# Kernel tuning notes

Hardware: AMD Instinct MI355X
Metric: run time of the kernel (lower is better)

The kernel has to match this reference:

```python
import jax, jax.numpy as jnp
import numpy as np

D_MODEL = 1024
N_HEADS = 16
HEAD_DIM = D_MODEL // N_HEADS


def setup_inputs() -> dict:
    key = jax.random.key(0)
    ks = jax.random.split(key, 10)
    s = 1.0 / np.sqrt(D_MODEL)
    inp = {
        "ts_features": jax.random.normal(ks[0], (8, 512, D_MODEL), dtype=jnp.float32),
        "llm_features": jax.random.normal(ks[1], (8, 2048, D_MODEL), dtype=jnp.float32),
        "q_w": jax.random.uniform(ks[2], (D_MODEL, D_MODEL), jnp.float32, -s, s),
        "q_b": jax.random.uniform(ks[3], (D_MODEL,), jnp.float32, -s, s),
        "k_w": jax.random.uniform(ks[4], (D_MODEL, D_MODEL), jnp.float32, -s, s),
        "k_b": jax.random.uniform(ks[5], (D_MODEL,), jnp.float32, -s, s),
        "v_w": jax.random.uniform(ks[6], (D_MODEL, D_MODEL), jnp.float32, -s, s),
        "v_b": jax.random.uniform(ks[7], (D_MODEL,), jnp.float32, -s, s),
        "o_w": jax.random.uniform(ks[8], (D_MODEL, D_MODEL), jnp.float32, -s, s),
        "o_b": jax.random.uniform(ks[9], (D_MODEL,), jnp.float32, -s, s),
    }
    return inp


def reference(ts_features, llm_features, q_w, q_b, k_w, k_b, v_w, v_b, o_w, o_b):
    B, P, _ = ts_features.shape
    S = llm_features.shape[1]
    # Linear projections (torch Linear: x @ W^T + b); split heads -> [B, H, L, Dh]
    q = (ts_features @ q_w.T + q_b).reshape(B, P, N_HEADS, HEAD_DIM).transpose(0, 2, 1, 3)
    k = (llm_features @ k_w.T + k_b).reshape(B, S, N_HEADS, HEAD_DIM).transpose(0, 2, 1, 3)
    v = (llm_features @ v_w.T + v_b).reshape(B, S, N_HEADS, HEAD_DIM).transpose(0, 2, 1, 3)
    # Full attention: scores [B, H, P, S]
    scores = jnp.einsum("bhpd,bhsd->bhps", q, k) / np.sqrt(HEAD_DIM).astype(np.float32)
    attn = jax.nn.softmax(scores, axis=-1)  # dropout is identity in eval mode
    context = jnp.einsum("bhps,bhsd->bhpd", attn, v)
    context = context.transpose(0, 2, 1, 3).reshape(B, P, D_MODEL)
    return context @ o_w.T + o_b
```

## Files before the change

### kernel.cpp

```cpp
#include <hip/hip_runtime.h>

#define DM 1024
#define B_ 8
#define P_ 512
#define S_ 2048

typedef __bf16 bf16;
typedef __bf16 bf16x4 __attribute__((ext_vector_type(4)));
typedef __bf16 bf16x8 __attribute__((ext_vector_type(8)));
typedef float f32x4 __attribute__((ext_vector_type(4)));
typedef float f32x16 __attribute__((ext_vector_type(16)));

__device__ __forceinline__ void gload_lds16(const void* g, void* l) {
  __builtin_amdgcn_global_load_lds(
      (const __attribute__((address_space(1))) unsigned int*)g,
      (__attribute__((address_space(3))) unsigned int*)l, 16, 0, 0);
}

__device__ __forceinline__ f32x4 mfma16(bf16x8 a, bf16x8 b, f32x4 c) {
  return __builtin_amdgcn_mfma_f32_16x16x32_bf16(a, b, c, 0, 0, 0);
}
__device__ __forceinline__ f32x16 mfma32(bf16x8 a, bf16x8 b, f32x16 c) {
  return __builtin_amdgcn_mfma_f32_32x32x16_bf16(a, b, c, 0, 0, 0);
}

__device__ __forceinline__ unsigned cvt_pk_bf16(float lo, float hi) {
  unsigned r;
  asm("v_cvt_pk_bf16_f32 %0, %1, %2" : "=v"(r) : "v"(lo), "v"(hi));
  return r;
}
__device__ __forceinline__ void plswap(unsigned& a, unsigned& b) {
  asm volatile("s_nop 1\n\tv_permlane32_swap_b32 %0, %1" : "+v"(a), "+v"(b));
}
__device__ __forceinline__ void bar() {
  asm volatile("" ::: "memory");
  __builtin_amdgcn_s_barrier();
  asm volatile("" ::: "memory");
}

union U8 { unsigned u[4]; bf16x8 v; };

#define QSCALE 0.18033688011112042f

__global__ void cvt_kernel(const float* __restrict__ in, bf16* __restrict__ out, int n4) {
  int i = blockIdx.x * blockDim.x + threadIdx.x;
  int stride = gridDim.x * blockDim.x;
  for (; i < n4; i += stride) {
    float4 v = reinterpret_cast<const float4*>(in)[i];
    bf16x4 o;
    o[0] = (bf16)v.x; o[1] = (bf16)v.y; o[2] = (bf16)v.z; o[3] = (bf16)v.w;
    reinterpret_cast<bf16x4*>(out)[i] = o;
  }
}

enum { MODE_F32 = 0, MODE_Q = 1, MODE_K = 2, MODE_VT = 3 };

template <int MODE>
__global__ __launch_bounds__(256) void gemm_bt(
    const bf16* __restrict__ A, const bf16* __restrict__ Bw,
    const float* __restrict__ bias, void* __restrict__ out) {
  __shared__ char As[16384];
  __shared__ char Bs[16384];
  const int tid = threadIdx.x;
  const int w = tid >> 6, lane = tid & 63;
  const int g = lane >> 4, l15 = lane & 15;
  const int tn = blockIdx.x, tm = blockIdx.y;
  const int wm = w >> 1, wn = w & 1;

  f32x4 acc[4][4] = {};

  const char* Abase = (const char*)A + (size_t)(tm * 128) * (DM * 2);
  const char* Bbase = (const char*)Bw + (size_t)(tn * 128) * (DM * 2);

  for (int kt = 0; kt < DM / 64; ++kt) {
#pragma unroll
    for (int i = 0; i < 4; ++i) {
      int f = (w * 4 + i) * 1024 + lane * 16;
      int row = f >> 7;
      int kb = f & 127;
      int src = kb ^ ((row & 7) << 4);
      gload_lds16(Abase + (size_t)row * (DM * 2) + kt * 128 + src, As + (w * 4 + i) * 1024);
      gload_lds16(Bbase + (size_t)row * (DM * 2) + kt * 128 + src, Bs + (w * 4 + i) * 1024);
    }
    __syncthreads();
#pragma unroll
    for (int kk = 0; kk < 2; ++kk) {
      bf16x8 af[4], bfr[4];
#pragma unroll
      for (int mi = 0; mi < 4; ++mi) {
        int row = wm * 64 + mi * 16 + l15;
        int off = row * 128 + ((kk * 64 + g * 16) ^ ((row & 7) << 4));
        af[mi] = *reinterpret_cast<const bf16x8*>(As + off);
      }
#pragma unroll
      for (int ni = 0; ni < 4; ++ni) {
        int row = wn * 64 + ni * 16 + l15;
        int off = row * 128 + ((kk * 64 + g * 16) ^ ((row & 7) << 4));
        bfr[ni] = *reinterpret_cast<const bf16x8*>(Bs + off);
      }
#pragma unroll
      for (int mi = 0; mi < 4; ++mi)
#pragma unroll
        for (int ni = 0; ni < 4; ++ni)
          acc[mi][ni] = mfma16(af[mi], bfr[ni], acc[mi][ni]);
    }
    __syncthreads();
  }

#pragma unroll
  for (int mi = 0; mi < 4; ++mi) {
#pragma unroll
    for (int ni = 0; ni < 4; ++ni) {
      const int n = tn * 128 + wn * 64 + ni * 16 + l15;
      const float bn = bias[n];
      const int mb = tm * 128 + wm * 64 + mi * 16 + g * 4;
#pragma unroll
      for (int r = 0; r < 4; ++r) {
        const int m = mb + r;
        const float v = acc[mi][ni][r] + bn;
        if constexpr (MODE == MODE_F32) {
          ((float*)out)[(size_t)m * 1024 + n] = v;
        } else {
          const int b = m >> 9, p = m & 511, h = n >> 6, d = n & 63;
          ((bf16*)out)[((size_t)((b * 16 + h) * 512 + p)) * 64 + d] = (bf16)(v * QSCALE);
        }
      }
    }
  }
}

template <int MODE>
__global__ __launch_bounds__(512, 2) void gemm256(
    const bf16* __restrict__ A, const bf16* __restrict__ Bw,
    const float* __restrict__ bias, void* __restrict__ out) {
  __shared__ char lds[131072];
  const int tid = threadIdx.x;
  const int w = tid >> 6, lane = tid & 63;
  const int g = lane >> 4, l15 = lane & 15;
  const int wm = w >> 2, wn = w & 3;

  const int id = blockIdx.x;
  const int nid = (id & 7) * 32 + (id >> 3);
  const int tn = nid & 3, tm = nid >> 2;

  const int f0 = tid * 16, f1 = f0 + 8192;
  const int r0 = f0 >> 7, r1 = f1 >> 7;
  const size_t so0 = (size_t)r0 * 2048 + ((f0 & 127) ^ ((r0 & 7) << 4));
  const size_t so1 = (size_t)r1 * 2048 + ((f1 & 127) ^ ((r1 & 7) << 4));

  const char* Ab = (const char*)A + (size_t)(tm * 256) * 2048;
  const char* Bb = (const char*)Bw + (size_t)(tn * 256) * 2048;

#define STG(OP, HALF, KT)                                                      \
  {                                                                            \
    const char* base = ((OP) ? Bb : Ab) + (size_t)((HALF) * 128) * 2048 +      \
                       (size_t)(KT) * 128;                                     \
    char* dst = lds + (OP) * 65536 + ((((KT) & 1) * 2 + (HALF)) * 16384);      \
    gload_lds16(base + so0, dst + f0);                                         \
    gload_lds16(base + so1, dst + f1);                                         \
  }

  f32x4 acc[8][4] = {};
  bf16x8 a[4][2], b0[2][2], b1[2][2];

#define RD_A(MH)                                                               \
  _Pragma("unroll") for (int mi = 0; mi < 4; ++mi) _Pragma("unroll")           \
      for (int kk = 0; kk < 2; ++kk) {                                         \
    int lr = (MH) * 64 + mi * 16 + l15;                                        \
    int off = (((unsigned)(kt & 1) * 2 + wm) * 16384) + lr * 128 +             \
              ((kk * 64 + g * 16) ^ ((lr & 7) << 4));                          \
    a[mi][kk] = *reinterpret_cast<const bf16x8*>(lds + off);                   \
  }
#define RD_B(NH, DST)                                                          \
  _Pragma("unroll") for (int ni = 0; ni < 2; ++ni) _Pragma("unroll")           \
      for (int kk = 0; kk < 2; ++kk) {                                         \
    int lr = (wn & 1) * 64 + ((NH) * 2 + ni) * 16 + l15;                       \
    int off = 65536 + (((unsigned)(kt & 1) * 2 + (wn >> 1)) * 16384) +         \
              lr * 128 + ((kk * 64 + g * 16) ^ ((lr & 7) << 4));               \
    DST[ni][kk] = *reinterpret_cast<const bf16x8*>(lds + off);                 \
  }
#define MM(MH, NH, B)                                                          \
  __builtin_amdgcn_s_setprio(1);                                              \
  _Pragma("unroll") for (int mi = 0; mi < 4; ++mi) _Pragma("unroll")           \
      for (int ni = 0; ni < 2; ++ni) _Pragma("unroll")                         \
      for (int kk = 0; kk < 2; ++kk)                                           \
          acc[(MH)*4 + mi][(NH)*2 + ni] =                                      \
              mfma16(a[mi][kk], B[ni][kk], acc[(MH)*4 + mi][(NH)*2 + ni]);     \
  __builtin_amdgcn_s_setprio(0);

  STG(0, 0, 0); STG(1, 0, 0); STG(0, 1, 0); STG(1, 1, 0);
  STG(1, 1, 1); STG(0, 0, 1); STG(1, 0, 1);
  asm volatile("s_waitcnt vmcnt(6)" ::: "memory");
  bar();

  for (int kt = 0; kt < 16; ++kt) {
    RD_A(0); RD_B(0, b0);
    if (kt + 1 < 16) STG(0, 1, kt + 1);
    bar();
    MM(0, 0, b0);
    bar();
    RD_B(1, b1);
    bar();
    MM(0, 1, b1);
    bar();
    RD_A(1);
    if (kt + 2 < 16) STG(1, 1, kt + 2);
    bar();
    MM(1, 0, b0);
    bar();
    if (kt + 2 < 16) { STG(0, 0, kt + 2); STG(1, 0, kt + 2); }
    if (kt < 14) {
      asm volatile("s_waitcnt vmcnt(6)" ::: "memory");
    } else {
      asm volatile("s_waitcnt vmcnt(0)" ::: "memory");
    }
    bar();
    MM(1, 1, b1);
    bar();
  }

#pragma unroll
  for (int am = 0; am < 8; ++am) {
#pragma unroll
    for (int an = 0; an < 4; ++an) {
      const int n = tn * 256 + wn * 64 + an * 16 + l15;
      const float bn = bias[n];
      const int mb = tm * 256 + wm * 128 + am * 16 + g * 4;
      const int h = n >> 6, d = n & 63;
      if constexpr (MODE == MODE_VT) {
        const int b = mb >> 11, s = mb & 2047;
        bf16x4 pk;
#pragma unroll
        for (int r = 0; r < 4; ++r) pk[r] = (bf16)(acc[am][an][r] + bn);
        *reinterpret_cast<bf16x4*>((bf16*)out + ((size_t)((b * 16 + h) * 64 + d)) * 2048 + s) = pk;
      } else {
#pragma unroll
        for (int r = 0; r < 4; ++r) {
          const int m = mb + r;
          const int b = m >> 11, s = m & 2047;
          ((bf16*)out)[((size_t)((b * 16 + h) * 2048 + s)) * 64 + d] =
              (bf16)(acc[am][an][r] + bn);
        }
      }
    }
  }
#undef STG
#undef RD_A
#undef RD_B
#undef MM
}

__global__ __launch_bounds__(256) void attn_kernel(
    const bf16* __restrict__ Q, const bf16* __restrict__ K,
    const bf16* __restrict__ VT, bf16* __restrict__ ctx) {
  __shared__ char lds[32768];
  const int tid = threadIdx.x;
  const int w = tid >> 6, lane = tid & 63;
  const int l31 = lane & 31, hi = lane >> 5;

  const int n = blockIdx.x;
  const int xcd = n & 7, mm = n >> 3;
  const int bh = xcd + ((mm >> 2) << 3);
  const int qt = mm & 3;
  const int q0 = qt * 128;

  const char* Kb = (const char*)(K + (size_t)bh * 2048 * 64);
  const char* Vb = (const char*)(VT + (size_t)bh * 64 * 2048);

  const char* Qrow = (const char*)(Q + ((size_t)bh * 512 + q0 + w * 32 + l31) * 64);
  bf16x8 qf[4];
#pragma unroll
  for (int kk = 0; kk < 4; ++kk)
    qf[kk] = *reinterpret_cast<const bf16x8*>(Qrow + kk * 32 + hi * 16);

  float lrun = 0.f;
  f32x16 oacc[2] = {};

#define STAGE(S0, BUF)                                                        \
  {                                                                           \
    _Pragma("unroll") for (int i = 0; i < 2; ++i) {                           \
      int f = i * 4096 + (w * 64 + lane) * 16;                                \
      int row = f >> 7, bb = f & 127;                                         \
      int src = bb ^ ((row & 7) << 4);                                        \
      gload_lds16(Kb + (size_t)((S0) + row) * 128 + src,                      \
                  (BUF) + i * 4096 + w * 1024);                               \
      gload_lds16(Vb + (size_t)row * 4096 + (size_t)(S0) * 2 + src,           \
                  (BUF) + 8192 + i * 4096 + w * 1024);                        \
    }                                                                         \
  }

  STAGE(0, lds);

  for (int c = 0; c < 32; ++c) {
    char* cur = lds + (c & 1) * 16384;
    if (c + 1 < 32) {
      STAGE((c + 1) * 64, lds + ((c + 1) & 1) * 16384);
      asm volatile("s_waitcnt vmcnt(4)" ::: "memory");
    } else {
      asm volatile("s_waitcnt vmcnt(0)" ::: "memory");
    }
    bar();

    f32x16 sa[2] = {};
    __builtin_amdgcn_s_setprio(1);
#pragma unroll
    for (int t = 0; t < 2; ++t) {
#pragma unroll
      for (int kk = 0; kk < 4; ++kk) {
        int row = t * 32 + l31;
        int off = row * 128 + ((kk * 32 + hi * 16) ^ ((row & 7) << 4));
        bf16x8 kf = *reinterpret_cast<const bf16x8*>(cur + off);
        sa[t] = mfma32(kf, qf[kk], sa[t]);
      }
    }
    __builtin_amdgcn_s_setprio(0);

    bf16x8 pf[4];
#pragma unroll
    for (int t = 0; t < 2; ++t)
#pragma unroll
      for (int h2 = 0; h2 < 2; ++h2) {
        float p[8];
#pragma unroll
        for (int j = 0; j < 8; ++j) {
          p[j] = __builtin_amdgcn_exp2f(sa[t][8 * h2 + j]);
          lrun += p[j];
        }
        unsigned a0 = cvt_pk_bf16(p[0], p[1]);
        unsigned a1 = cvt_pk_bf16(p[2], p[3]);
        unsigned a2 = cvt_pk_bf16(p[4], p[5]);
        unsigned a3 = cvt_pk_bf16(p[6], p[7]);
        plswap(a0, a2);
        plswap(a1, a3);
        U8 u;
        u.u[0] = a0; u.u[1] = a1; u.u[2] = a2; u.u[3] = a3;
        pf[t * 2 + h2] = u.v;
      }

    __builtin_amdgcn_s_setprio(1);
#pragma unroll
    for (int dt = 0; dt < 2; ++dt) {
#pragma unroll
      for (int ks = 0; ks < 4; ++ks) {
        int row = dt * 32 + l31;
        int off = 8192 + row * 128 + ((ks * 32 + hi * 16) ^ ((row & 7) << 4));
        bf16x8 vf = *reinterpret_cast<const bf16x8*>(cur + off);
        oacc[dt] = mfma32(vf, pf[ks], oacc[dt]);
      }
    }
    __builtin_amdgcn_s_setprio(0);
    bar();
  }

  lrun += __shfl_xor(lrun, 32);
  const float inv = 1.0f / lrun;
  const int b = bh >> 4, h = bh & 15;
  const int prow = q0 + w * 32 + l31;
  bf16* dst = ctx + ((size_t)(b * 512 + prow)) * 1024 + h * 64;
#pragma unroll
  for (int dt = 0; dt < 2; ++dt)
#pragma unroll
    for (int g4 = 0; g4 < 4; ++g4) {
      bf16x4 pk4;
#pragma unroll
      for (int r = 0; r < 4; ++r) pk4[r] = (bf16)(oacc[dt][g4 * 4 + r] * inv);
      *reinterpret_cast<bf16x4*>(dst + dt * 32 + g4 * 8 + hi * 4) = pk4;
    }
#undef STAGE
}

extern "C" void kernel_launch(void* const* d_in, const int* in_sizes, int n_in,
                              void* d_out, int out_size, void* d_ws, size_t ws_size,
                              hipStream_t stream) {
  const float* ts = (const float*)d_in[0];
  const float* llm = (const float*)d_in[1];
  const float* qw = (const float*)d_in[2];
  const float* qb = (const float*)d_in[3];
  const float* kw = (const float*)d_in[4];
  const float* kb = (const float*)d_in[5];
  const float* vw = (const float*)d_in[6];
  const float* vb = (const float*)d_in[7];
  const float* ow = (const float*)d_in[8];
  const float* ob = (const float*)d_in[9];

  char* ws = (char*)d_ws;
  bf16* ts_bf = (bf16*)(ws + (0ull << 20));
  bf16* llm_bf = (bf16*)(ws + (8ull << 20));
  bf16* qw_bf = (bf16*)(ws + (40ull << 20));
  bf16* kw_bf = (bf16*)(ws + (42ull << 20));
  bf16* vw_bf = (bf16*)(ws + (44ull << 20));
  bf16* ow_bf = (bf16*)(ws + (46ull << 20));
  bf16* Qb = (bf16*)(ws + (48ull << 20));
  bf16* Kb = (bf16*)(ws + (56ull << 20));
  bf16* VTb = (bf16*)(ws + (88ull << 20));
  bf16* ctx = (bf16*)(ws + (120ull << 20));

  cvt_kernel<<<2048, 256, 0, stream>>>(ts, ts_bf, (B_ * P_ * DM) / 4);
  cvt_kernel<<<2048, 256, 0, stream>>>(llm, llm_bf, (B_ * S_ * DM) / 4);
  cvt_kernel<<<1024, 256, 0, stream>>>(qw, qw_bf, (DM * DM) / 4);
  cvt_kernel<<<1024, 256, 0, stream>>>(kw, kw_bf, (DM * DM) / 4);
  cvt_kernel<<<1024, 256, 0, stream>>>(vw, vw_bf, (DM * DM) / 4);
  cvt_kernel<<<1024, 256, 0, stream>>>(ow, ow_bf, (DM * DM) / 4);

  gemm_bt<MODE_Q><<<dim3(8, 32), 256, 0, stream>>>(ts_bf, qw_bf, qb, Qb);
  gemm256<MODE_K><<<256, 512, 0, stream>>>(llm_bf, kw_bf, kb, Kb);
  gemm256<MODE_VT><<<256, 512, 0, stream>>>(llm_bf, vw_bf, vb, VTb);
  attn_kernel<<<512, 256, 0, stream>>>(Qb, Kb, VTb, ctx);
  gemm_bt<MODE_F32><<<dim3(8, 32), 256, 0, stream>>>(ctx, ow_bf, ob, (void*)d_out);
}
```

Before: 200.0 us.

## Split attention KV range in two and merge partials in a combine kernel

Each attention block now handles half of the 2048-key sequence, which doubles the grid from 512 to 1024 blocks for better CU fill. Instead of normalised bf16 context, each block writes unnormalised fp32 partial outputs and row sums. A new combine kernel adds the two halves, divides by the summed denominators and writes the bf16 context. The gain in parallelism is paid for with an extra launch and about 32 MB of fp32 partials written and read back through workspace that overlaps the already-consumed input buffers. The merge relies on both halves using the same softmax offset, since no per-half max rescaling is applied.

Result: slower. 208.7 us (+4.4%).

```diff
diff --git a/kernel.cpp b/kernel.cpp
--- a/kernel.cpp
+++ b/kernel.cpp
@@ -252,17 +252,20 @@
 
 __global__ __launch_bounds__(256) void attn_kernel(
     const bf16* __restrict__ Q, const bf16* __restrict__ K,
-    const bf16* __restrict__ VT, bf16* __restrict__ ctx) {
+    const bf16* __restrict__ VT, float* __restrict__ Opart,
+    float* __restrict__ lpart) {
   __shared__ char lds[32768];
   const int tid = threadIdx.x;
   const int w = tid >> 6, lane = tid & 63;
   const int l31 = lane & 31, hi = lane >> 5;
 
   const int n = blockIdx.x;
-  const int xcd = n & 7, mm = n >> 3;
-  const int bh = xcd + ((mm >> 2) << 3);
-  const int qt = mm & 3;
+  const int wid = (n & 7) * 128 + (n >> 3);
+  const int bh = wid >> 3;
+  const int qt = (wid >> 1) & 3;
+  const int sh = wid & 1;
   const int q0 = qt * 128;
+  const int sbase = sh * 1024;
 
   const char* Kb = (const char*)(K + (size_t)bh * 2048 * 64);
   const char* Vb = (const char*)(VT + (size_t)bh * 64 * 2048);
@@ -289,12 +292,12 @@
     }                                                                         \
   }
 
-  STAGE(0, lds);
-
-  for (int c = 0; c < 32; ++c) {
+  STAGE(sbase, lds);
+
+  for (int c = 0; c < 16; ++c) {
     char* cur = lds + (c & 1) * 16384;
-    if (c + 1 < 32) {
-      STAGE((c + 1) * 64, lds + ((c + 1) & 1) * 16384);
+    if (c + 1 < 16) {
+      STAGE(sbase + (c + 1) * 64, lds + ((c + 1) & 1) * 16384);
       asm volatile("s_waitcnt vmcnt(4)" ::: "memory");
     } else {
       asm volatile("s_waitcnt vmcnt(0)" ::: "memory");
@@ -353,20 +356,47 @@
   }
 
   lrun += __shfl_xor(lrun, 32);
-  const float inv = 1.0f / lrun;
-  const int b = bh >> 4, h = bh & 15;
   const int prow = q0 + w * 32 + l31;
-  bf16* dst = ctx + ((size_t)(b * 512 + prow)) * 1024 + h * 64;
+  const size_t rowg = (size_t)bh * 512 + prow;
+  float* Od = Opart + ((size_t)sh * 65536 + rowg) * 64;
+  if (hi == 0) lpart[(size_t)sh * 65536 + rowg] = lrun;
 #pragma unroll
   for (int dt = 0; dt < 2; ++dt)
 #pragma unroll
     for (int g4 = 0; g4 < 4; ++g4) {
-      bf16x4 pk4;
-#pragma unroll
-      for (int r = 0; r < 4; ++r) pk4[r] = (bf16)(oacc[dt][g4 * 4 + r] * inv);
-      *reinterpret_cast<bf16x4*>(dst + dt * 32 + g4 * 8 + hi * 4) = pk4;
+      f32x4 st;
+#pragma unroll
+      for (int r = 0; r < 4; ++r) st[r] = oacc[dt][g4 * 4 + r];
+      *reinterpret_cast<f32x4*>(Od + dt * 32 + g4 * 8 + hi * 4) = st;
     }
 #undef STAGE
+}
+
+__global__ __launch_bounds__(256) void combine_kernel(
+    const float* __restrict__ Opart, const float* __restrict__ lpart,
+    bf16* __restrict__ ctx) {
+  int idx = blockIdx.x * blockDim.x + threadIdx.x;
+  int row = idx >> 3, dc = (idx & 7) * 8;
+  const float* o0 = Opart + (size_t)row * 64 + dc;
+  const float* o1 = o0 + (size_t)65536 * 64;
+  float inv = 1.0f / (lpart[row] + lpart[65536 + row]);
+  float4 a0 = *(const float4*)o0;
+  float4 a1 = *(const float4*)(o0 + 4);
+  float4 c0 = *(const float4*)o1;
+  float4 c1 = *(const float4*)(o1 + 4);
+  int bh = row >> 9, p = row & 511;
+  int b = bh >> 4, h = bh & 15;
+  bf16* dst = ctx + ((size_t)(b * 512 + p)) * 1024 + h * 64 + dc;
+  bf16x8 o;
+  o[0] = (bf16)((a0.x + c0.x) * inv);
+  o[1] = (bf16)((a0.y + c0.y) * inv);
+  o[2] = (bf16)((a0.z + c0.z) * inv);
+  o[3] = (bf16)((a0.w + c0.w) * inv);
+  o[4] = (bf16)((a1.x + c1.x) * inv);
+  o[5] = (bf16)((a1.y + c1.y) * inv);
+  o[6] = (bf16)((a1.z + c1.z) * inv);
+  o[7] = (bf16)((a1.w + c1.w) * inv);
+  *reinterpret_cast<bf16x8*>(dst) = o;
 }
 
 extern "C" void kernel_launch(void* const* d_in, const int* in_sizes, int n_in,
@@ -394,6 +424,8 @@
   bf16* Kb = (bf16*)(ws + (56ull << 20));
   bf16* VTb = (bf16*)(ws + (88ull << 20));
   bf16* ctx = (bf16*)(ws + (120ull << 20));
+  float* Opart = (float*)(ws + (0ull << 20));
+  float* lpart = (float*)(ws + (32ull << 20));
 
   cvt_kernel<<<2048, 256, 0, stream>>>(ts, ts_bf, (B_ * P_ * DM) / 4);
   cvt_kernel<<<2048, 256, 0, stream>>>(llm, llm_bf, (B_ * S_ * DM) / 4);
@@ -405,6 +437,7 @@
   gemm_bt<MODE_Q><<<dim3(8, 32), 256, 0, stream>>>(ts_bf, qw_bf, qb, Qb);
   gemm256<MODE_K><<<256, 512, 0, stream>>>(llm_bf, kw_bf, kb, Kb);
   gemm256<MODE_VT><<<256, 512, 0, stream>>>(llm_bf, vw_bf, vb, VTb);
-  attn_kernel<<<512, 256, 0, stream>>>(Qb, Kb, VTb, ctx);
+  attn_kernel<<<1024, 256, 0, stream>>>(Qb, Kb, VTb, Opart, lpart);
+  combine_kernel<<<2048, 256, 0, stream>>>(Opart, lpart, ctx);
   gemm_bt<MODE_F32><<<dim3(8, 32), 256, 0, stream>>>(ctx, ow_bf, ob, (void*)d_out);
 }
```

## Fuse conversion kernels and make attention single-wave with direct register loads

Applied to the files above, without the earlier changes.

The six fp32-to-bf16 conversion launches become one kernel that picks its source tensor by index range, which cuts launch overhead. The attention kernel moves from 4-wave blocks that share K/V tiles in LDS, with barriers, to one-wave blocks of 32 query rows. Each wave loads K and V fragments straight from global memory into registers, prefetching the next K chunk during the PV MFMAs. This removes the barriers and the LDS traffic, but each wave now fetches K/V on its own, so global and L2 traffic rises fourfold and latency hiding relies on occupancy.

Measured after the change: 259.0 us. 1.3x slower.

```diff
diff --git a/kernel.cpp b/kernel.cpp
--- a/kernel.cpp
+++ b/kernel.cpp
@@ -42,14 +42,30 @@
 
 #define QSCALE 0.18033688011112042f
 
-__global__ void cvt_kernel(const float* __restrict__ in, bf16* __restrict__ out, int n4) {
+__global__ void cvt_all(const float* __restrict__ ts, const float* __restrict__ llm,
+                        const float* __restrict__ qw, const float* __restrict__ kw,
+                        const float* __restrict__ vw, const float* __restrict__ ow,
+                        bf16* __restrict__ ts_o, bf16* __restrict__ llm_o,
+                        bf16* __restrict__ qw_o, bf16* __restrict__ kw_o,
+                        bf16* __restrict__ vw_o, bf16* __restrict__ ow_o) {
+  const int total = 24 << 18;
   int i = blockIdx.x * blockDim.x + threadIdx.x;
-  int stride = gridDim.x * blockDim.x;
-  for (; i < n4; i += stride) {
-    float4 v = reinterpret_cast<const float4*>(in)[i];
+  const int stride = gridDim.x * blockDim.x;
+  for (; i < total; i += stride) {
+    int r = i >> 18;
+    const float* in;
+    bf16* out;
+    int off;
+    if (r < 4) { in = ts; out = ts_o; off = i; }
+    else if (r < 20) { in = llm; out = llm_o; off = i - (4 << 18); }
+    else if (r == 20) { in = qw; out = qw_o; off = i - (20 << 18); }
+    else if (r == 21) { in = kw; out = kw_o; off = i - (21 << 18); }
+    else if (r == 22) { in = vw; out = vw_o; off = i - (22 << 18); }
+    else { in = ow; out = ow_o; off = i - (23 << 18); }
+    float4 v = reinterpret_cast<const float4*>(in)[off];
     bf16x4 o;
     o[0] = (bf16)v.x; o[1] = (bf16)v.y; o[2] = (bf16)v.z; o[3] = (bf16)v.w;
-    reinterpret_cast<bf16x4*>(out)[i] = o;
+    reinterpret_cast<bf16x4*>(out)[off] = o;
   }
 }
 
@@ -250,24 +266,22 @@
 #undef MM
 }
 
-__global__ __launch_bounds__(256) void attn_kernel(
+__global__ __launch_bounds__(64, 2) void attn_kernel(
     const bf16* __restrict__ Q, const bf16* __restrict__ K,
     const bf16* __restrict__ VT, bf16* __restrict__ ctx) {
-  __shared__ char lds[32768];
-  const int tid = threadIdx.x;
-  const int w = tid >> 6, lane = tid & 63;
+  const int lane = threadIdx.x;
   const int l31 = lane & 31, hi = lane >> 5;
 
   const int n = blockIdx.x;
-  const int xcd = n & 7, mm = n >> 3;
-  const int bh = xcd + ((mm >> 2) << 3);
-  const int qt = mm & 3;
-  const int q0 = qt * 128;
+  const int wid = (n & 7) * 256 + (n >> 3);
+  const int bh = wid >> 4;
+  const int qt = wid & 15;
+  const int q0 = qt * 32;
 
   const char* Kb = (const char*)(K + (size_t)bh * 2048 * 64);
   const char* Vb = (const char*)(VT + (size_t)bh * 64 * 2048);
 
-  const char* Qrow = (const char*)(Q + ((size_t)bh * 512 + q0 + w * 32 + l31) * 64);
+  const char* Qrow = (const char*)(Q + ((size_t)bh * 512 + q0 + l31) * 64);
   bf16x8 qf[4];
 #pragma unroll
   for (int kk = 0; kk < 4; ++kk)
@@ -275,45 +289,30 @@
 
   float lrun = 0.f;
   f32x16 oacc[2] = {};
-
-#define STAGE(S0, BUF)                                                        \
-  {                                                                           \
-    _Pragma("unroll") for (int i = 0; i < 2; ++i) {                           \
-      int f = i * 4096 + (w * 64 + lane) * 16;                                \
-      int row = f >> 7, bb = f & 127;                                         \
-      int src = bb ^ ((row & 7) << 4);                                        \
-      gload_lds16(Kb + (size_t)((S0) + row) * 128 + src,                      \
-                  (BUF) + i * 4096 + w * 1024);                               \
-      gload_lds16(Vb + (size_t)row * 4096 + (size_t)(S0) * 2 + src,           \
-                  (BUF) + 8192 + i * 4096 + w * 1024);                        \
-    }                                                                         \
-  }
-
-  STAGE(0, lds);
+  bf16x8 kf[8], vf[8];
+
+#define LDK(C)                                                                \
+  _Pragma("unroll") for (int t = 0; t < 2; ++t) _Pragma("unroll")             \
+      for (int kk = 0; kk < 4; ++kk)                                          \
+          kf[t * 4 + kk] = *reinterpret_cast<const bf16x8*>(                  \
+              Kb + (size_t)((C) * 64 + t * 32 + l31) * 128 + kk * 32 + hi * 16);
+#define LDV(C)                                                                \
+  _Pragma("unroll") for (int dt = 0; dt < 2; ++dt) _Pragma("unroll")          \
+      for (int ks = 0; ks < 4; ++ks)                                          \
+          vf[dt * 4 + ks] = *reinterpret_cast<const bf16x8*>(                 \
+              Vb + (size_t)(dt * 32 + l31) * 4096 + (C) * 128 + ks * 32 +     \
+              hi * 16);
+
+  LDK(0);
 
   for (int c = 0; c < 32; ++c) {
-    char* cur = lds + (c & 1) * 16384;
-    if (c + 1 < 32) {
-      STAGE((c + 1) * 64, lds + ((c + 1) & 1) * 16384);
-      asm volatile("s_waitcnt vmcnt(4)" ::: "memory");
-    } else {
-      asm volatile("s_waitcnt vmcnt(0)" ::: "memory");
-    }
-    bar();
+    LDV(c);
 
     f32x16 sa[2] = {};
-    __builtin_amdgcn_s_setprio(1);
-#pragma unroll
-    for (int t = 0; t < 2; ++t) {
-#pragma unroll
-      for (int kk = 0; kk < 4; ++kk) {
-        int row = t * 32 + l31;
-        int off = row * 128 + ((kk * 32 + hi * 16) ^ ((row & 7) << 4));
-        bf16x8 kf = *reinterpret_cast<const bf16x8*>(cur + off);
-        sa[t] = mfma32(kf, qf[kk], sa[t]);
-      }
-    }
-    __builtin_amdgcn_s_setprio(0);
+#pragma unroll
+    for (int t = 0; t < 2; ++t)
+#pragma unroll
+      for (int kk = 0; kk < 4; ++kk) sa[t] = mfma32(kf[t * 4 + kk], qf[kk], sa[t]);
 
     bf16x8 pf[4];
 #pragma unroll
@@ -337,25 +336,19 @@
         pf[t * 2 + h2] = u.v;
       }
 
-    __builtin_amdgcn_s_setprio(1);
-#pragma unroll
-    for (int dt = 0; dt < 2; ++dt) {
-#pragma unroll
-      for (int ks = 0; ks < 4; ++ks) {
-        int row = dt * 32 + l31;
-        int off = 8192 + row * 128 + ((ks * 32 + hi * 16) ^ ((row & 7) << 4));
-        bf16x8 vf = *reinterpret_cast<const bf16x8*>(cur + off);
-        oacc[dt] = mfma32(vf, pf[ks], oacc[dt]);
-      }
-    }
-    __builtin_amdgcn_s_setprio(0);
-    bar();
+    if (c + 1 < 32) LDK(c + 1);
+
+#pragma unroll
+    for (int dt = 0; dt < 2; ++dt)
+#pragma unroll
+      for (int ks = 0; ks < 4; ++ks)
+        oacc[dt] = mfma32(vf[dt * 4 + ks], pf[ks], oacc[dt]);
   }
 
   lrun += __shfl_xor(lrun, 32);
   const float inv = 1.0f / lrun;
   const int b = bh >> 4, h = bh & 15;
-  const int prow = q0 + w * 32 + l31;
+  const int prow = q0 + l31;
   bf16* dst = ctx + ((size_t)(b * 512 + prow)) * 1024 + h * 64;
 #pragma unroll
   for (int dt = 0; dt < 2; ++dt)
@@ -366,7 +359,8 @@
       for (int r = 0; r < 4; ++r) pk4[r] = (bf16)(oacc[dt][g4 * 4 + r] * inv);
       *reinterpret_cast<bf16x4*>(dst + dt * 32 + g4 * 8 + hi * 4) = pk4;
     }
-#undef STAGE
+#undef LDK
+#undef LDV
 }
 
 extern "C" void kernel_launch(void* const* d_in, const int* in_sizes, int n_in,
@@ -395,16 +389,12 @@
   bf16* VTb = (bf16*)(ws + (88ull << 20));
   bf16* ctx = (bf16*)(ws + (120ull << 20));
 
-  cvt_kernel<<<2048, 256, 0, stream>>>(ts, ts_bf, (B_ * P_ * DM) / 4);
-  cvt_kernel<<<2048, 256, 0, stream>>>(llm, llm_bf, (B_ * S_ * DM) / 4);
-  cvt_kernel<<<1024, 256, 0, stream>>>(qw, qw_bf, (DM * DM) / 4);
-  cvt_kernel<<<1024, 256, 0, stream>>>(kw, kw_bf, (DM * DM) / 4);
-  cvt_kernel<<<1024, 256, 0, stream>>>(vw, vw_bf, (DM * DM) / 4);
-  cvt_kernel<<<1024, 256, 0, stream>>>(ow, ow_bf, (DM * DM) / 4);
+  cvt_all<<<2048, 256, 0, stream>>>(ts, llm, qw, kw, vw, ow,
+                                    ts_bf, llm_bf, qw_bf, kw_bf, vw_bf, ow_bf);
 
   gemm_bt<MODE_Q><<<dim3(8, 32), 256, 0, stream>>>(ts_bf, qw_bf, qb, Qb);
   gemm256<MODE_K><<<256, 512, 0, stream>>>(llm_bf, kw_bf, kb, Kb);
   gemm256<MODE_VT><<<256, 512, 0, stream>>>(llm_bf, vw_bf, vb, VTb);
-  attn_kernel<<<512, 256, 0, stream>>>(Qb, Kb, VTb, ctx);
+  attn_kernel<<<2048, 64, 0, stream>>>(Qb, Kb, VTb, ctx);
   gemm_bt<MODE_F32><<<dim3(8, 32), 256, 0, stream>>>(ctx, ow_bf, ob, (void*)d_out);
 }
```

## Fuse input conversions into one kernel and merge K/V projections into one GEMM

Applied to the files above, without the earlier changes.

Replaces six separate fp32-to-bf16 conversion launches with a single kernel that dispatches by index range over all inputs. The K and V projection GEMMs become one 512-block launch that treats the K and V weights as one N=2048 matrix and splits the epilogue by column to write K or transposed V. This relies on kw_bf and vw_bf sitting next to each other in the workspace (42MB and 44MB, each 2MB). It cuts launch overhead and tail effects and improves occupancy for the projections, at the cost of a branchy conversion loop.

After: 197.4 us. About the same (-1.3%).

```diff
diff --git a/kernel.cpp b/kernel.cpp
--- a/kernel.cpp
+++ b/kernel.cpp
@@ -42,18 +42,34 @@
 
 #define QSCALE 0.18033688011112042f
 
-__global__ void cvt_kernel(const float* __restrict__ in, bf16* __restrict__ out, int n4) {
+__global__ void cvt_all(const float* __restrict__ ts, const float* __restrict__ llm,
+                        const float* __restrict__ qw, const float* __restrict__ kw,
+                        const float* __restrict__ vw, const float* __restrict__ ow,
+                        bf16* __restrict__ ts_o, bf16* __restrict__ llm_o,
+                        bf16* __restrict__ qw_o, bf16* __restrict__ kw_o,
+                        bf16* __restrict__ vw_o, bf16* __restrict__ ow_o) {
+  const int total = 24 << 18;
   int i = blockIdx.x * blockDim.x + threadIdx.x;
-  int stride = gridDim.x * blockDim.x;
-  for (; i < n4; i += stride) {
-    float4 v = reinterpret_cast<const float4*>(in)[i];
+  const int stride = gridDim.x * blockDim.x;
+  for (; i < total; i += stride) {
+    int r = i >> 18;
+    const float* in;
+    bf16* out;
+    int off;
+    if (r < 4) { in = ts; out = ts_o; off = i; }
+    else if (r < 20) { in = llm; out = llm_o; off = i - (4 << 18); }
+    else if (r == 20) { in = qw; out = qw_o; off = i - (20 << 18); }
+    else if (r == 21) { in = kw; out = kw_o; off = i - (21 << 18); }
+    else if (r == 22) { in = vw; out = vw_o; off = i - (22 << 18); }
+    else { in = ow; out = ow_o; off = i - (23 << 18); }
+    float4 v = reinterpret_cast<const float4*>(in)[off];
     bf16x4 o;
     o[0] = (bf16)v.x; o[1] = (bf16)v.y; o[2] = (bf16)v.z; o[3] = (bf16)v.w;
-    reinterpret_cast<bf16x4*>(out)[i] = o;
-  }
-}
-
-enum { MODE_F32 = 0, MODE_Q = 1, MODE_K = 2, MODE_VT = 3 };
+    reinterpret_cast<bf16x4*>(out)[off] = o;
+  }
+}
+
+enum { MODE_F32 = 0, MODE_Q = 1 };
 
 template <int MODE>
 __global__ __launch_bounds__(256) void gemm_bt(
@@ -129,10 +145,10 @@
   }
 }
 
-template <int MODE>
-__global__ __launch_bounds__(512, 2) void gemm256(
+__global__ __launch_bounds__(512, 2) void gemm256kv(
     const bf16* __restrict__ A, const bf16* __restrict__ Bw,
-    const float* __restrict__ bias, void* __restrict__ out) {
+    const float* __restrict__ kb, const float* __restrict__ vb,
+    bf16* __restrict__ Kout, bf16* __restrict__ VTout) {
   __shared__ char lds[131072];
   const int tid = threadIdx.x;
   const int w = tid >> 6, lane = tid & 63;
@@ -140,8 +156,8 @@
   const int wm = w >> 2, wn = w & 3;
 
   const int id = blockIdx.x;
-  const int nid = (id & 7) * 32 + (id >> 3);
-  const int tn = nid & 3, tm = nid >> 2;
+  const int nid = (id & 7) * 64 + (id >> 3);
+  const int tn = nid & 7, tm = nid >> 3;
 
   const int f0 = tid * 16, f1 = f0 + 8192;
   const int r0 = f0 >> 7, r1 = f1 >> 7;
@@ -224,23 +240,22 @@
 #pragma unroll
     for (int an = 0; an < 4; ++an) {
       const int n = tn * 256 + wn * 64 + an * 16 + l15;
-      const float bn = bias[n];
       const int mb = tm * 256 + wm * 128 + am * 16 + g * 4;
-      const int h = n >> 6, d = n & 63;
-      if constexpr (MODE == MODE_VT) {
-        const int b = mb >> 11, s = mb & 2047;
+      const int b = mb >> 11, s = mb & 2047;
+      if (n >= 1024) {
+        const int h = (n - 1024) >> 6, d = (n - 1024) & 63;
+        const float bn = vb[n - 1024];
         bf16x4 pk;
 #pragma unroll
         for (int r = 0; r < 4; ++r) pk[r] = (bf16)(acc[am][an][r] + bn);
-        *reinterpret_cast<bf16x4*>((bf16*)out + ((size_t)((b * 16 + h) * 64 + d)) * 2048 + s) = pk;
+        *reinterpret_cast<bf16x4*>(VTout + ((size_t)((b * 16 + h) * 64 + d)) * 2048 + s) = pk;
       } else {
-#pragma unroll
-        for (int r = 0; r < 4; ++r) {
-          const int m = mb + r;
-          const int b = m >> 11, s = m & 2047;
-          ((bf16*)out)[((size_t)((b * 16 + h) * 2048 + s)) * 64 + d] =
+        const int h = n >> 6, d = n & 63;
+        const float bn = kb[n];
+#pragma unroll
+        for (int r = 0; r < 4; ++r)
+          Kout[((size_t)((b * 16 + h) * 2048 + s + r)) * 64 + d] =
               (bf16)(acc[am][an][r] + bn);
-        }
       }
     }
   }
@@ -395,16 +410,11 @@
   bf16* VTb = (bf16*)(ws + (88ull << 20));
   bf16* ctx = (bf16*)(ws + (120ull << 20));
 
-  cvt_kernel<<<2048, 256, 0, stream>>>(ts, ts_bf, (B_ * P_ * DM) / 4);
-  cvt_kernel<<<2048, 256, 0, stream>>>(llm, llm_bf, (B_ * S_ * DM) / 4);
-  cvt_kernel<<<1024, 256, 0, stream>>>(qw, qw_bf, (DM * DM) / 4);
-  cvt_kernel<<<1024, 256, 0, stream>>>(kw, kw_bf, (DM * DM) / 4);
-  cvt_kernel<<<1024, 256, 0, stream>>>(vw, vw_bf, (DM * DM) / 4);
-  cvt_kernel<<<1024, 256, 0, stream>>>(ow, ow_bf, (DM * DM) / 4);
+  cvt_all<<<2048, 256, 0, stream>>>(ts, llm, qw, kw, vw, ow,
+                                    ts_bf, llm_bf, qw_bf, kw_bf, vw_bf, ow_bf);
 
   gemm_bt<MODE_Q><<<dim3(8, 32), 256, 0, stream>>>(ts_bf, qw_bf, qb, Qb);
-  gemm256<MODE_K><<<256, 512, 0, stream>>>(llm_bf, kw_bf, kb, Kb);
-  gemm256<MODE_VT><<<256, 512, 0, stream>>>(llm_bf, vw_bf, vb, VTb);
+  gemm256kv<<<512, 512, 0, stream>>>(llm_bf, kw_bf, kb, vb, Kb, VTb);
   attn_kernel<<<512, 256, 0, stream>>>(Qb, Kb, VTb, ctx);
   gemm_bt<MODE_F32><<<dim3(8, 32), 256, 0, stream>>>(ctx, ow_bf, ob, (void*)d_out);
 }
```
